# Kernel tuning notes

Hardware: AMD Instinct MI355X
Metric: run time of the kernel (lower is better)

The kernel has to match this reference:

```python
import jax, jax.numpy as jnp
import numpy as np

NEG_SLOPE = 0.2  # LeakyReLU slope of the conv activation


def setup_inputs() -> dict:
    key = jax.random.key(0)
    k1, k2, k3, k4 = jax.random.split(key, 4)
    B, N, F, G, S, D = 32, 1024, 512, 16, 64, 256
    x = jax.random.normal(k1, (B, N, F), dtype=jnp.float32)
    # irregular per-group index sets: random permutation of positions, 16 groups of 64
    idx = jax.random.permutation(k2, N).reshape(G, S).astype(jnp.int32)
    # per-group Dense weights (HeNormal-like scale) and biases
    W = jax.random.normal(k3, (G, F, D), dtype=jnp.float32) * np.float32(np.sqrt(2.0 / F))
    b = jnp.zeros((G, D), dtype=jnp.float32)
    # Conv1D(512 filters, kernel=32, valid), weights in WIO layout
    conv_w = jax.random.normal(k4, (32, D, 512), dtype=jnp.float32) * np.float32(np.sqrt(2.0 / (32 * D)))
    conv_b = jnp.zeros((512,), dtype=jnp.float32)
    return {"x": x, "idx": idx, "W": W, "b": b, "conv_w": conv_w, "conv_b": conv_b}


def reference(x, idx, W, b, conv_w, conv_b):
    # per-group gather: [B, G, S, F]
    xg = x[:, idx, :]
    # per-group Dense (grouped GEMM): [B, G, S, D]
    out = jnp.einsum('bgsf,gfd->bgsd', xg, W) + b[None, :, None, :]
    B, G, S, D = out.shape
    # concat groups along position axis: [B, G*S, D]
    out = out.reshape(B, G * S, D)
    # dropout is identity at inference (training=False)
    # Conv1D(512, kernel=32, valid) + LeakyReLU(0.2)
    y = jax.lax.conv_general_dilated(
        out, conv_w, window_strides=(1,), padding='VALID',
        dimension_numbers=('NWC', 'WIO', 'NWC'))
    y = y + conv_b
    return jnp.where(y >= 0, y, NEG_SLOPE * y)
```

## Files before the change

### kernel.cpp

```cpp
#include <hip/hip_runtime.h>
#include <stdint.h>


typedef __bf16  bf16x8 __attribute__((ext_vector_type(8)));
typedef float   f32x4  __attribute__((ext_vector_type(4)));

__device__ __forceinline__ uint16_t f2bf(float f) {
    union { float f; uint32_t u; } x; x.f = f;
    uint32_t r = x.u + 0x7FFFu + ((x.u >> 16) & 1u);
    return (uint16_t)(r >> 16);
}
template <typename T>
__device__ __forceinline__ void gl2lds16(const T* g, T* l) {
    __builtin_amdgcn_global_load_lds(
        (const __attribute__((address_space(1))) uint32_t*)g,
        (__attribute__((address_space(3))) uint32_t*)l, 16, 0, 0);
}

__global__ void transpose_cvt(const float* __restrict__ in, uint16_t* __restrict__ out,
                              int R, int C) {
    __shared__ float tile[32][33];
    const float* inm = in + (size_t)blockIdx.z * R * C;
    uint16_t* outm = out + (size_t)blockIdx.z * R * C;
    int c0 = blockIdx.x * 32, r0 = blockIdx.y * 32;
    int tx = threadIdx.x, ty = threadIdx.y;
    #pragma unroll
    for (int i = 0; i < 32; i += 8)
        tile[ty + i][tx] = inm[(size_t)(r0 + ty + i) * C + (c0 + tx)];
    __syncthreads();
    #pragma unroll
    for (int i = 0; i < 32; i += 8)
        outm[(size_t)(c0 + ty + i) * R + (r0 + tx)] = f2bf(tile[tx][ty + i]);
}

__global__ __launch_bounds__(256, 2)
void k_group_gemm(const float*    __restrict__ x,
                  const int*      __restrict__ idx,
                  const uint16_t* __restrict__ Wt,
                  const float*    __restrict__ bias,
                  uint16_t*       __restrict__ interm) {
    __shared__ float    smemA[128 * 64];
    __shared__ uint16_t smemB[128 * 64];
    __shared__ int sidx[64];
    const int tid  = threadIdx.x;
    const int g    = blockIdx.z;
    const int bp   = blockIdx.y;
    const int n0   = blockIdx.x * 128;
    const int wave = tid >> 6, lane = tid & 63;
    const int quad = lane >> 4, l15 = lane & 15;
    const int mw = (wave & 1) * 64, nw = (wave >> 1) * 64;

    if (tid < 64) sidx[tid] = idx[g * 64 + tid];
    __syncthreads();

    uint32_t aoffF[8];
    #pragma unroll
    for (int is = 0; is < 8; ++is) {
        int r = wave * 32 + is * 4 + (lane >> 4);
        int b = bp * 2 + (r >> 6), s = r & 63;
        int gc = (lane & 15) ^ (r & 15);
        aoffF[is] = ((uint32_t)b * 1024u + (uint32_t)sidx[s]) * 512u + (uint32_t)gc * 4u;
    }
    uint32_t boff[4];
    #pragma unroll
    for (int is = 0; is < 4; ++is) {
        int r = wave * 32 + is * 8 + (lane >> 3);
        int gc8 = ((lane & 7) ^ (lane >> 3)) * 8;
        boff[is] = ((uint32_t)(g * 256 + n0 + r)) * 512u + (uint32_t)gc8;
    }

    f32x4 acc[4][4];
    #pragma unroll
    for (int i = 0; i < 4; ++i)
        #pragma unroll
        for (int j = 0; j < 4; ++j)
            #pragma unroll
            for (int c = 0; c < 4; ++c) acc[i][j][c] = 0.f;

    for (int kb = 0; kb < 8; ++kb) {
        #pragma unroll
        for (int is = 0; is < 8; ++is)
            gl2lds16(x + aoffF[is] + kb * 64, &smemA[(wave * 32 + is * 4) * 64]);
        #pragma unroll
        for (int is = 0; is < 4; ++is)
            gl2lds16(Wt + boff[is] + kb * 64, &smemB[(wave * 32 + is * 8) * 64]);
        __syncthreads();
        #pragma unroll
        for (int ks = 0; ks < 2; ++ks) {
            const int kc = ks * 4 + quad;
            bf16x8 af[4], bfr[4];
            #pragma unroll
            for (int i = 0; i < 4; ++i) {
                int m = mw + i * 16 + l15;
                int s0 = (2 * kc) ^ (m & 15);
                int s1 = (2 * kc + 1) ^ (m & 15);
                f32x4 f0 = *(const f32x4*)&smemA[m * 64 + s0 * 4];
                f32x4 f1 = *(const f32x4*)&smemA[m * 64 + s1 * 4];
                #pragma unroll
                for (int j = 0; j < 4; ++j) { af[i][j] = (__bf16)f0[j]; af[i][j + 4] = (__bf16)f1[j]; }
            }
            #pragma unroll
            for (int j = 0; j < 4; ++j) {
                int n = nw + j * 16 + l15;
                bfr[j] = *(const bf16x8*)&smemB[(n * 8 + (kc ^ (n & 7))) * 8];
            }
            #pragma unroll
            for (int i = 0; i < 4; ++i)
                #pragma unroll
                for (int j = 0; j < 4; ++j)
                    acc[i][j] = __builtin_amdgcn_mfma_f32_16x16x32_bf16(af[i], bfr[j], acc[i][j], 0, 0, 0);
        }
        __syncthreads();
    }

    #pragma unroll
    for (int j = 0; j < 4; ++j) {
        int col = n0 + nw + j * 16 + l15;
        float bv = bias[g * 256 + col];
        #pragma unroll
        for (int i = 0; i < 4; ++i) {
            int mbase = mw + i * 16 + quad * 4;
            #pragma unroll
            for (int r = 0; r < 4; ++r) {
                int m = mbase + r;
                int b = bp * 2 + (m >> 6), s = m & 63;
                interm[((size_t)b * 1024 + g * 64 + s) * 256 + col] = f2bf(acc[i][j][r] + bv);
            }
        }
    }
}

__global__ __launch_bounds__(256, 2)
void k_conv_gemm(const uint16_t* __restrict__ interm,
                 const uint16_t* __restrict__ cwT,
                 const float*    __restrict__ cb,
                 float*          __restrict__ y) {
    __shared__ uint16_t smem[8192 + 16384];
    const int tid  = threadIdx.x;
    const int n0   = blockIdx.z * 256;
    const int t0   = blockIdx.y * 128;
    const int nb   = blockIdx.x;
    const int wave = tid >> 6, lane = tid & 63;
    const int quad = lane >> 4, l15 = lane & 15;
    const int mw = (wave & 1) * 64;
    const int nw = (wave >> 1) * 128;

    const int l8r = lane >> 3;
    const int gc8 = ((lane & 7) ^ l8r) * 8;

    uint32_t aoff[4], boff[8];
    #pragma unroll
    for (int is = 0; is < 4; ++is) {
        int r = wave * 32 + is * 8 + l8r;
        aoff[is] = ((uint32_t)(nb * 1024 + t0 + r)) * 256u + gc8;
    }
    #pragma unroll
    for (int is = 0; is < 8; ++is) {
        int r = wave * 64 + is * 8 + l8r;
        boff[is] = ((uint32_t)(n0 + r)) * 8192u + gc8;
    }

    f32x4 acc[4][8];
    #pragma unroll
    for (int i = 0; i < 4; ++i)
        #pragma unroll
        for (int j = 0; j < 8; ++j)
            #pragma unroll
            for (int c = 0; c < 4; ++c) acc[i][j][c] = 0.f;

    for (int kb = 0; kb < 128; ++kb) {
        const int k  = kb >> 2;
        const int c0 = (kb & 3) * 64;
        #pragma unroll
        for (int is = 0; is < 4; ++is)
            gl2lds16(interm + aoff[is] + (uint32_t)k * 256u + c0,
                     &smem[(wave * 32 + is * 8) * 64]);
        #pragma unroll
        for (int is = 0; is < 8; ++is)
            gl2lds16(cwT + boff[is] + (uint32_t)kb * 64u,
                     &smem[8192 + (wave * 64 + is * 8) * 64]);
        __syncthreads();
        #pragma unroll
        for (int ks = 0; ks < 2; ++ks) {
            const int kc = ks * 4 + quad;
            bf16x8 af[4], bfr[8];
            #pragma unroll
            for (int i = 0; i < 4; ++i) {
                int m = mw + i * 16 + l15;
                af[i] = *(const bf16x8*)&smem[(m * 8 + (kc ^ (m & 7))) * 8];
            }
            #pragma unroll
            for (int j = 0; j < 8; ++j) {
                int n = nw + j * 16 + l15;
                bfr[j] = *(const bf16x8*)&smem[8192 + (n * 8 + (kc ^ (n & 7))) * 8];
            }
            #pragma unroll
            for (int i = 0; i < 4; ++i)
                #pragma unroll
                for (int j = 0; j < 8; ++j)
                    acc[i][j] = __builtin_amdgcn_mfma_f32_16x16x32_bf16(af[i], bfr[j], acc[i][j], 0, 0, 0);
        }
        __syncthreads();
    }

    #pragma unroll
    for (int j = 0; j < 8; ++j) {
        int col = n0 + nw + j * 16 + l15;
        float bv = cb[col];
        #pragma unroll
        for (int i = 0; i < 4; ++i) {
            int tb = t0 + mw + i * 16 + quad * 4;
            #pragma unroll
            for (int r = 0; r < 4; ++r) {
                int t = tb + r;
                if (t < 993) {
                    float v = acc[i][j][r] + bv;
                    v = (v >= 0.f) ? v : 0.2f * v;
                    y[((size_t)nb * 993 + t) * 512 + col] = v;
                }
            }
        }
    }
}

extern "C" void kernel_launch(void* const* d_in, const int* in_sizes, int n_in,
                              void* d_out, int out_size, void* d_ws, size_t ws_size,
                              hipStream_t stream) {
    const float* x   = (const float*)d_in[0];
    const int*   idx = (const int*)  d_in[1];
    const float* W   = (const float*)d_in[2];
    const float* b   = (const float*)d_in[3];
    const float* cw  = (const float*)d_in[4];
    const float* cb  = (const float*)d_in[5];
    float* out = (float*)d_out;

    uint16_t* interm = (uint16_t*)d_ws;
    uint16_t* Wt  = interm + (size_t)32832 * 256;
    uint16_t* cwT = Wt + (size_t)16 * 256 * 512;

    transpose_cvt<<<dim3(256 / 32, 512 / 32, 16), dim3(32, 8), 0, stream>>>(W, Wt, 512, 256);
    transpose_cvt<<<dim3(512 / 32, 8192 / 32, 1), dim3(32, 8), 0, stream>>>(cw, cwT, 8192, 512);

    k_group_gemm<<<dim3(2, 16, 16), 256, 0, stream>>>(x, idx, Wt, b, interm);
    k_conv_gemm <<<dim3(32, 8, 2),  256, 0, stream>>>(interm, cwT, cb, out);
}
```

Baseline: 381.1 us.

## Register-prefetch gathered A tiles, convert to bf16 before LDS, swap grid order

The grouped GEMM no longer gathers fp32 rows of x straight into LDS with direct loads. It loads them into registers one k-block ahead, converts them to bf16, and writes them to a halved, swizzled bf16 LDS tile, so the fp32-to-bf16 conversion is done once instead of per MFMA fragment. The global fetch of the next k-block overlaps with the current compute, and LDS usage drops. The grid axes are also swapped so blocks sharing a group and batch pair are scheduled in a different order, which changes cache reuse of W versus x. In exchange the kernel holds more registers for the prefetch buffers and adds extra syncs per k-block.

```diff
diff --git a/kernel.cpp b/kernel.cpp
--- a/kernel.cpp
+++ b/kernel.cpp
@@ -39,13 +39,13 @@
                   const uint16_t* __restrict__ Wt,
                   const float*    __restrict__ bias,
                   uint16_t*       __restrict__ interm) {
-    __shared__ float    smemA[128 * 64];
-    __shared__ uint16_t smemB[128 * 64];
+    __shared__ uint16_t smemA[8192];
+    __shared__ uint16_t smemB[8192];
     __shared__ int sidx[64];
     const int tid  = threadIdx.x;
+    const int bp   = blockIdx.x;
+    const int n0   = blockIdx.y * 128;
     const int g    = blockIdx.z;
-    const int bp   = blockIdx.y;
-    const int n0   = blockIdx.x * 128;
     const int wave = tid >> 6, lane = tid & 63;
     const int quad = lane >> 4, l15 = lane & 15;
     const int mw = (wave & 1) * 64, nw = (wave >> 1) * 64;
@@ -53,21 +53,43 @@
     if (tid < 64) sidx[tid] = idx[g * 64 + tid];
     __syncthreads();
 
-    uint32_t aoffF[8];
-    #pragma unroll
-    for (int is = 0; is < 8; ++is) {
-        int r = wave * 32 + is * 4 + (lane >> 4);
+    const int l8r = lane >> 3;
+    const int gc8 = ((lane & 7) ^ l8r) * 8;
+
+    uint32_t aoffF[4], boff[4];
+    #pragma unroll
+    for (int is = 0; is < 4; ++is) {
+        int r = wave * 32 + is * 8 + l8r;
         int b = bp * 2 + (r >> 6), s = r & 63;
-        int gc = (lane & 15) ^ (r & 15);
-        aoffF[is] = ((uint32_t)b * 1024u + (uint32_t)sidx[s]) * 512u + (uint32_t)gc * 4u;
-    }
-    uint32_t boff[4];
-    #pragma unroll
-    for (int is = 0; is < 4; ++is) {
-        int r = wave * 32 + is * 8 + (lane >> 3);
-        int gc8 = ((lane & 7) ^ (lane >> 3)) * 8;
-        boff[is] = ((uint32_t)(g * 256 + n0 + r)) * 512u + (uint32_t)gc8;
-    }
+        aoffF[is] = ((uint32_t)b * 1024u + (uint32_t)sidx[s]) * 512u + (uint32_t)gc8;
+        boff[is]  = ((uint32_t)(g * 256 + n0 + r)) * 512u + (uint32_t)gc8;
+    }
+
+    auto loadA = [&](int kb, f32x4* dst) {
+        #pragma unroll
+        for (int is = 0; is < 4; ++is) {
+            const float* p = x + aoffF[is] + (uint32_t)kb * 64u;
+            dst[2 * is]     = *(const f32x4*)p;
+            dst[2 * is + 1] = *(const f32x4*)(p + 4);
+        }
+    };
+    auto stageA = [&](const f32x4* src) {
+        #pragma unroll
+        for (int is = 0; is < 4; ++is) {
+            bf16x8 o;
+            #pragma unroll
+            for (int j = 0; j < 4; ++j) {
+                o[j]     = (__bf16)src[2 * is][j];
+                o[j + 4] = (__bf16)src[2 * is + 1][j];
+            }
+            *(bf16x8*)&smemA[(wave * 32 + is * 8 + l8r) * 64 + (lane & 7) * 8] = o;
+        }
+    };
+    auto stageB = [&](int kb) {
+        #pragma unroll
+        for (int is = 0; is < 4; ++is)
+            gl2lds16(Wt + boff[is] + (uint32_t)kb * 64u, &smemB[(wave * 32 + is * 8) * 64]);
+    };
 
     f32x4 acc[4][4];
     #pragma unroll
@@ -77,14 +99,7 @@
             #pragma unroll
             for (int c = 0; c < 4; ++c) acc[i][j][c] = 0.f;
 
-    for (int kb = 0; kb < 8; ++kb) {
-        #pragma unroll
-        for (int is = 0; is < 8; ++is)
-            gl2lds16(x + aoffF[is] + kb * 64, &smemA[(wave * 32 + is * 4) * 64]);
-        #pragma unroll
-        for (int is = 0; is < 4; ++is)
-            gl2lds16(Wt + boff[is] + kb * 64, &smemB[(wave * 32 + is * 8) * 64]);
-        __syncthreads();
+    auto compute = [&]() {
         #pragma unroll
         for (int ks = 0; ks < 2; ++ks) {
             const int kc = ks * 4 + quad;
@@ -92,12 +107,7 @@
             #pragma unroll
             for (int i = 0; i < 4; ++i) {
                 int m = mw + i * 16 + l15;
-                int s0 = (2 * kc) ^ (m & 15);
-                int s1 = (2 * kc + 1) ^ (m & 15);
-                f32x4 f0 = *(const f32x4*)&smemA[m * 64 + s0 * 4];
-                f32x4 f1 = *(const f32x4*)&smemA[m * 64 + s1 * 4];
-                #pragma unroll
-                for (int j = 0; j < 4; ++j) { af[i][j] = (__bf16)f0[j]; af[i][j + 4] = (__bf16)f1[j]; }
+                af[i] = *(const bf16x8*)&smemA[(m * 8 + (kc ^ (m & 7))) * 8];
             }
             #pragma unroll
             for (int j = 0; j < 4; ++j) {
@@ -110,6 +120,22 @@
                 for (int j = 0; j < 4; ++j)
                     acc[i][j] = __builtin_amdgcn_mfma_f32_16x16x32_bf16(af[i], bfr[j], acc[i][j], 0, 0, 0);
         }
+    };
+
+    f32x4 a0[8], a1[8];
+    loadA(0, a0);
+    #pragma unroll
+    for (int kp = 0; kp < 4; ++kp) {
+        const int kb = kp * 2;
+        stageA(a0); stageB(kb);
+        loadA(kb + 1, a1);
+        __syncthreads();
+        compute();
+        __syncthreads();
+        stageA(a1); stageB(kb + 1);
+        if (kb + 2 < 8) loadA(kb + 2, a0);
+        __syncthreads();
+        compute();
         __syncthreads();
     }
 
@@ -241,6 +267,6 @@
     transpose_cvt<<<dim3(256 / 32, 512 / 32, 16), dim3(32, 8), 0, stream>>>(W, Wt, 512, 256);
     transpose_cvt<<<dim3(512 / 32, 8192 / 32, 1), dim3(32, 8), 0, stream>>>(cw, cwT, 8192, 512);
 
-    k_group_gemm<<<dim3(2, 16, 16), 256, 0, stream>>>(x, idx, Wt, b, interm);
+    k_group_gemm<<<dim3(16, 2, 16), 256, 0, stream>>>(x, idx, Wt, b, interm);
     k_conv_gemm <<<dim3(32, 8, 2),  256, 0, stream>>>(interm, cwT, cb, out);
 }
```

Measured after the change: 369.4 us (median of 2 runs). 3.1% less time.
